# Performance work log

Measured on AMD Instinct MI355X. Metric: run time of the kernel, lower is better.

## Reference

```python
import jax, jax.numpy as jnp
import numpy as np

N_PTILES = 4096
MAX_SOURCES = 1
PTILE_SLEN = 53  # odd -> slen == ptile_slen, size_lens is identity
N_BANDS = 1


def setup_inputs() -> dict:
    key = jax.random.key(0)
    k1, k2, k3, k4, k5, k6 = jax.random.split(key, 6)
    shape = (N_PTILES, MAX_SOURCES)
    gal = jax.random.uniform(k1, shape + (7,), dtype=jnp.float32)
    # realistic SIE lens params per _sample_lens_params: b in [5,30], q in (0,1)
    b = jax.random.uniform(k2, shape + (1,), dtype=jnp.float32) * 25.0 + 5.0
    centers = jax.random.normal(k3, shape + (2,), dtype=jnp.float32)
    q = jax.random.uniform(k4, shape + (1,), dtype=jnp.float32) * 0.8 + 0.1
    beta = (jax.random.uniform(k5, shape + (1,), dtype=jnp.float32) - 0.5) * (np.pi / 2)
    ellf = (1.0 - q) / (1.0 + q)
    e1 = ellf * jnp.cos(beta)
    e2 = ellf * jnp.sin(beta)
    lens_params = jnp.concatenate([gal, b, centers, e1, e2], axis=-1)  # [..., 12]
    bools = (jax.random.uniform(k6, shape + (1,), dtype=jnp.float32) < 0.7).astype(jnp.float32)
    return {"lens_params": lens_params, "lensed_galaxy_bools": bools}


def _render_unlensed(gal_p, slen):
    # Differentiable Gaussian stand-in for the (CPU galsim) unlensed source render.
    c = jnp.arange(slen, dtype=jnp.float32) - (slen - 1) / 2.0
    yy, xx = jnp.meshgrid(c, c, indexing="ij")
    flux = gal_p[:, 0] * 1000.0 + 100.0      # [N]
    sigma = gal_p[:, 3] * 3.0 + 1.0          # [N]
    r2 = xx[None] ** 2 + yy[None] ** 2       # [1, S, S]
    s2 = (sigma ** 2)[:, None, None]
    return flux[:, None, None] * jnp.exp(-0.5 * r2 / s2) / (2.0 * np.pi * s2)


def _sie_deflection(x, y, lens_p):
    # x, y: [1, S, S]; lens_p: [N, 5] -> (xg, yg): [N, S, S]
    b, cx, cy, e1, e2 = [lens_p[:, i][:, None, None] for i in range(5)]
    ell = jnp.sqrt(e1 ** 2 + e2 ** 2)
    q = (1.0 - ell) / (1.0 + ell)
    phirad = jnp.arctan(e2 / e1)
    cosp, sinp = jnp.cos(phirad), jnp.sin(phirad)
    xsie = (x - cx) * cosp + (y - cy) * sinp
    ysie = (y - cy) * cosp - (x - cx) * sinp
    r_ell = jnp.sqrt(q * xsie ** 2 + ysie ** 2 / q + 1e-12)
    qfact = jnp.sqrt(1.0 / q - q)
    eps = 0.001
    safe = jnp.maximum(qfact, eps)
    denom = r_ell + (r_ell == 0)
    xtg = jnp.where(qfact >= eps, b / safe * jnp.arctan(safe * xsie / denom), b * xsie / denom)
    ytg = jnp.where(qfact >= eps, b / safe * jnp.arctanh(safe * ysie / denom), b * ysie / denom)
    xg = xtg * cosp - ytg * sinp
    yg = ytg * cosp + xtg * sinp
    return xg, yg


def _bilinear(im, xs, ys):
    # im: [N, S, S]; xs (col coord), ys (row coord): [N, S, S]
    N, S, _ = im.shape
    x0 = jnp.clip(jnp.floor(xs).astype(jnp.int32), 0, S - 1)
    x1 = jnp.clip(jnp.floor(xs).astype(jnp.int32) + 1, 0, S - 1)
    y0 = jnp.clip(jnp.floor(ys).astype(jnp.int32), 0, S - 1)
    y1 = jnp.clip(jnp.floor(ys).astype(jnp.int32) + 1, 0, S - 1)
    flat = im.reshape(N, S * S)

    def g(yi, xi):
        return jnp.take_along_axis(flat, (yi * S + xi).reshape(N, -1), axis=1).reshape(N, S, S)

    x0f, x1f = x0.astype(im.dtype), x1.astype(im.dtype)
    y0f, y1f = y0.astype(im.dtype), y1.astype(im.dtype)
    # weights use the CLIPPED integer corners, matching bilinear_interpolate_numpy
    wa = (x1f - xs) * (y1f - ys)
    wb = (x1f - xs) * (ys - y0f)
    wc = (xs - x0f) * (y1f - ys)
    wd = (xs - x0f) * (ys - y0f)
    return g(y0, x0) * wa + g(y1, x0) * wb + g(y0, x1) * wc + g(y1, x1) * wd


def _forward(lens_params, lensed_galaxy_bools):
    n_ptiles, max_s, P = lens_params.shape
    z = lens_params.reshape(-1, P)
    gal_p, lens_p = z[:, :7], z[:, 7:]
    slen = PTILE_SLEN
    unlensed = _render_unlensed(gal_p, slen)            # [N, S, S]
    # grid exactly as lens_galsim: range [-nx//2, nx//2] over nx points
    nx = slen
    lo = float((-nx) // 2)   # -27 for nx=53
    hi = float(nx // 2)      # 26
    coords = (hi - lo) * jnp.arange(nx, dtype=jnp.float32) / (nx - 1) + lo
    x = jnp.broadcast_to(coords[None, :], (nx, nx))  # varies along columns
    y = jnp.broadcast_to(coords[:, None], (nx, nx))  # varies along rows
    xg, yg = _sie_deflection(x[None], y[None], lens_p)
    shift = float(nx // 2)
    lensed = _bilinear(unlensed, x[None] - xg + shift, y[None] - yg + shift)
    out = lensed.reshape(n_ptiles, max_s, N_BANDS, slen, slen)
    # render-all + mask is equivalent to the zeros-init + boolean-fill + final mask
    return out * lensed_galaxy_bools[..., None, None]


def reference(lens_params, lensed_galaxy_bools):
    return _forward(lens_params, lensed_galaxy_bools)
```

## Files before the change

### kernel.cpp

```cpp
#include <hip/hip_runtime.h>
#include <math.h>

#define SLEN 53
#define NPIX 2809
#define NPARAM 12
#define BLK 256
#define NSLOT 11

__device__ __forceinline__ float fast_atan(float u) {
    float t = __builtin_fabsf(u);
    float rin = __builtin_amdgcn_rcpf(t);
    bool big = t > 1.0f;
    float w = big ? rin : t;
    float z = w * w;
    float p = -0.01172120f;
    p = __builtin_fmaf(p, z,  0.05265332f);
    p = __builtin_fmaf(p, z, -0.11643287f);
    p = __builtin_fmaf(p, z,  0.19354346f);
    p = __builtin_fmaf(p, z, -0.33262347f);
    p = __builtin_fmaf(p, z,  0.99997726f);
    float r = w * p;
    r = big ? 1.57079632679489662f - r : r;
    return __builtin_copysignf(r, u);
}

__device__ __forceinline__ float fast_atanh(float v) {
    float a = __builtin_fabsf(v);
    float t = (1.0f + a) * __builtin_amdgcn_rcpf(1.0f - a);
    float r = 0.34657359027997264f * __builtin_amdgcn_logf(t);
    return __builtin_copysignf(r, v);
}

__global__ __launch_bounds__(BLK) void lgtd_kernel(
    const float* __restrict__ lens_params,
    const float* __restrict__ bools,
    float* __restrict__ out)
{
    __shared__ float Etab[SLEN + 3];
    const int tile = blockIdx.x;
    float* outp = out + (size_t)tile * NPIX;
    const int tid = threadIdx.x;

    const float bl = bools[tile];
    if (bl == 0.0f) {
        #pragma unroll
        for (int s = 0; s < NSLOT; ++s) {
            const int idx = s * BLK + tid;
            if (s < NSLOT - 1 || idx < NPIX) outp[idx] = 0.0f;
        }
        return;
    }

    const float* p = lens_params + tile * NPARAM;
    const float flux = __builtin_fmaf(p[0], 1000.0f, 100.0f);
    const float sg   = __builtin_fmaf(p[3], 3.0f, 1.0f);
    const float s2   = sg * sg;
    const float rs2  = __builtin_amdgcn_rcpf(s2);
    const float A    = flux * 0.15915494309189533577f * rs2;
    const float nh2  = -0.72134752044448170368f * rs2;
    const float b  = p[7], cx = p[8], cy = p[9], e1 = p[10], e2 = p[11];
    const float rell = __builtin_amdgcn_rsqf(__builtin_fmaf(e1, e1, e2 * e2));
    const float cosp = e1 * rell;
    const float sinp = e2 * rell;
    const float ell  = __builtin_fmaf(e1, cosp, e2 * sinp);
    const float q    = (1.0f - ell) * __builtin_amdgcn_rcpf(1.0f + ell);
    const float qinv = __builtin_amdgcn_rcpf(q);
    const float qf   = __builtin_amdgcn_sqrtf(qinv - q);
    const float safe = fmaxf(qf, 0.001f);
    const float bos  = b * __builtin_amdgcn_rcpf(safe);
    const bool  mb   = (qf >= 0.001f);

    const float sA = __builtin_amdgcn_sqrtf(A * bl);
    if (tid < SLEN) {
        const float d = (float)tid - 26.0f;
        Etab[tid] = sA * __builtin_amdgcn_exp2f((nh2 * d) * d);
    }
    __syncthreads();

    const float KC = 1.019230769230769231f;
    #pragma unroll
    for (int s = 0; s < NSLOT; ++s) {
        int idx = s * BLK + tid;
        if (s == NSLOT - 1) idx = min(idx, NPIX - 1);
        const unsigned i = ((unsigned)idx * 39569u) >> 21;
        const int j = idx - (int)i * 53;
        const float xc = __builtin_fmaf((float)j, KC, -27.0f);
        const float yc = __builtin_fmaf((float)i, KC, -27.0f);

        const float dx = xc - cx, dy = yc - cy;
        const float xsie = __builtin_fmaf(dx, cosp, dy * sinp);
        const float ysie = __builtin_fmaf(dy, cosp, -dx * sinp);
        const float arg  = __builtin_fmaf(q * xsie, xsie,
                           __builtin_fmaf(qinv * ysie, ysie, 1e-12f));
        const float rcp_r = __builtin_amdgcn_rsqf(arg);
        float xtg, ytg;
        if (mb) {
            const float srr = safe * rcp_r;
            xtg = bos * fast_atan(srr * xsie);
            ytg = bos * fast_atanh(srr * ysie);
        } else {
            const float brr = b * rcp_r;
            xtg = brr * xsie;
            ytg = brr * ysie;
        }
        const float xg = __builtin_fmaf(xtg, cosp, -ytg * sinp);
        const float yg = __builtin_fmaf(ytg, cosp,  xtg * sinp);

        const float xs = (xc + 26.0f) - xg;
        const float ys = (yc + 26.0f) - yg;
        const float fx = __builtin_floorf(xs);
        const float fy = __builtin_floorf(ys);
        const float x0f = fminf(fmaxf(fx,        0.0f), 52.0f);
        const float x1f = fminf(fmaxf(fx + 1.0f, 0.0f), 52.0f);
        const float y0f = fminf(fmaxf(fy,        0.0f), 52.0f);
        const float y1f = fminf(fmaxf(fy + 1.0f, 0.0f), 52.0f);

        const float Ex0 = Etab[(int)x0f];
        const float Ex1 = Etab[(int)x1f];
        const float Ey0 = Etab[(int)y0f];
        const float Ey1 = Etab[(int)y1f];

        const float Fx = __builtin_fmaf(x1f - xs, Ex0, (xs - x0f) * Ex1);
        const float Fy = __builtin_fmaf(y1f - ys, Ey0, (ys - y0f) * Ey1);
        outp[idx] = Fx * Fy;
    }
}

extern "C" void kernel_launch(void* const* d_in, const int* in_sizes, int n_in,
                              void* d_out, int out_size, void* d_ws, size_t ws_size,
                              hipStream_t stream) {
    const float* lens  = (const float*)d_in[0];
    const float* bools = (const float*)d_in[1];
    float* out = (float*)d_out;
    const int n_tiles = in_sizes[1];
    lgtd_kernel<<<n_tiles, BLK, 0, stream>>>(lens, bools, out);
}
```

Baseline: 82.69 us.

## Process four tiles per block to amortize setup and share pixel coordinates

Each block now handles four tiles instead of one, with per-tile lens parameters held in register arrays and a four-row shared Gaussian table. The pixel index, row/column and coordinate math are computed once per pixel and reused across the four tiles. This cuts the block count fourfold and spreads per-block setup and sync over more work. In exchange the per-tile branch on zero masks moves inside the inner loop, the outer slot loop is no longer unrolled, register pressure rises, and fewer blocks are available to fill the GPU.

```diff
diff --git a/kernel.cpp b/kernel.cpp
--- a/kernel.cpp
+++ b/kernel.cpp
@@ -5,7 +5,9 @@
 #define NPIX 2809
 #define NPARAM 12
 #define BLK 256
+#define TPB 4
 #define NSLOT 11
+#define KC 1.019230769230769231f
 
 __device__ __forceinline__ float fast_atan(float u) {
     float t = __builtin_fabsf(u);
@@ -34,95 +36,132 @@
 __global__ __launch_bounds__(BLK) void lgtd_kernel(
     const float* __restrict__ lens_params,
     const float* __restrict__ bools,
-    float* __restrict__ out)
+    float* __restrict__ out, int n_tiles)
 {
-    __shared__ float Etab[SLEN + 3];
-    const int tile = blockIdx.x;
-    float* outp = out + (size_t)tile * NPIX;
+    __shared__ float Etab[TPB][SLEN];
+    const int base = blockIdx.x * TPB;
     const int tid = threadIdx.x;
 
-    const float bl = bools[tile];
-    if (bl == 0.0f) {
+    float blv[TPB];
+    bool  val[TPB];
+    bool  any = false;
+    #pragma unroll
+    for (int t = 0; t < TPB; ++t) {
+        val[t] = (base + t < n_tiles);
+        blv[t] = val[t] ? bools[base + t] : 0.0f;
+        any = any || (blv[t] != 0.0f);
+    }
+    if (!any) {
         #pragma unroll
-        for (int s = 0; s < NSLOT; ++s) {
-            const int idx = s * BLK + tid;
-            if (s < NSLOT - 1 || idx < NPIX) outp[idx] = 0.0f;
+        for (int t = 0; t < TPB; ++t) {
+            if (!val[t]) continue;
+            float* outp = out + (size_t)(base + t) * NPIX;
+            #pragma unroll 1
+            for (int s = 0; s < NSLOT; ++s)
+                outp[min(s * BLK + tid, NPIX - 1)] = 0.0f;
         }
         return;
     }
 
-    const float* p = lens_params + tile * NPARAM;
-    const float flux = __builtin_fmaf(p[0], 1000.0f, 100.0f);
-    const float sg   = __builtin_fmaf(p[3], 3.0f, 1.0f);
-    const float s2   = sg * sg;
-    const float rs2  = __builtin_amdgcn_rcpf(s2);
-    const float A    = flux * 0.15915494309189533577f * rs2;
-    const float nh2  = -0.72134752044448170368f * rs2;
-    const float b  = p[7], cx = p[8], cy = p[9], e1 = p[10], e2 = p[11];
-    const float rell = __builtin_amdgcn_rsqf(__builtin_fmaf(e1, e1, e2 * e2));
-    const float cosp = e1 * rell;
-    const float sinp = e2 * rell;
-    const float ell  = __builtin_fmaf(e1, cosp, e2 * sinp);
-    const float q    = (1.0f - ell) * __builtin_amdgcn_rcpf(1.0f + ell);
-    const float qinv = __builtin_amdgcn_rcpf(q);
-    const float qf   = __builtin_amdgcn_sqrtf(qinv - q);
-    const float safe = fmaxf(qf, 0.001f);
-    const float bos  = b * __builtin_amdgcn_rcpf(safe);
-    const bool  mb   = (qf >= 0.001f);
+    float cospv[TPB], sinpv[TPB], qv[TPB], qinvv[TPB], safev[TPB],
+          bosv[TPB], cxv[TPB], cyv[TPB], bv[TPB], nh2v[TPB], sAv[TPB];
+    bool  mbv[TPB];
+    #pragma unroll
+    for (int t = 0; t < TPB; ++t) {
+        if (blv[t] == 0.0f) {
+            cospv[t]=1.0f; sinpv[t]=0.0f; qv[t]=1.0f; qinvv[t]=1.0f;
+            safev[t]=1.0f; bosv[t]=0.0f; cxv[t]=0.0f; cyv[t]=0.0f;
+            bv[t]=0.0f; nh2v[t]=0.0f; sAv[t]=0.0f; mbv[t]=true;
+            continue;
+        }
+        const float* p = lens_params + (size_t)(base + t) * NPARAM;
+        const float flux = __builtin_fmaf(p[0], 1000.0f, 100.0f);
+        const float sg   = __builtin_fmaf(p[3], 3.0f, 1.0f);
+        const float s2   = sg * sg;
+        const float rs2  = __builtin_amdgcn_rcpf(s2);
+        const float A    = flux * 0.15915494309189533577f * rs2;
+        nh2v[t] = -0.72134752044448170368f * rs2;
+        bv[t] = p[7]; cxv[t] = p[8]; cyv[t] = p[9];
+        const float e1 = p[10], e2 = p[11];
+        const float rell = __builtin_amdgcn_rsqf(__builtin_fmaf(e1, e1, e2 * e2));
+        const float cosp = e1 * rell;
+        const float sinp = e2 * rell;
+        cospv[t] = cosp; sinpv[t] = sinp;
+        const float ell  = __builtin_fmaf(e1, cosp, e2 * sinp);
+        const float q    = (1.0f - ell) * __builtin_amdgcn_rcpf(1.0f + ell);
+        qv[t] = q;
+        const float qinv = __builtin_amdgcn_rcpf(q);
+        qinvv[t] = qinv;
+        const float qf   = __builtin_amdgcn_sqrtf(qinv - q);
+        const float safe = fmaxf(qf, 0.001f);
+        safev[t] = safe;
+        bosv[t]  = bv[t] * __builtin_amdgcn_rcpf(safe);
+        mbv[t]   = (qf >= 0.001f);
+        sAv[t]   = __builtin_amdgcn_sqrtf(A * blv[t]);
+    }
 
-    const float sA = __builtin_amdgcn_sqrtf(A * bl);
     if (tid < SLEN) {
-        const float d = (float)tid - 26.0f;
-        Etab[tid] = sA * __builtin_amdgcn_exp2f((nh2 * d) * d);
+        const float d  = (float)tid - 26.0f;
+        const float d2 = d * d;
+        #pragma unroll
+        for (int t = 0; t < TPB; ++t)
+            Etab[t][tid] = sAv[t] * __builtin_amdgcn_exp2f(nh2v[t] * d2);
     }
     __syncthreads();
 
-    const float KC = 1.019230769230769231f;
-    #pragma unroll
+    #pragma unroll 1
     for (int s = 0; s < NSLOT; ++s) {
-        int idx = s * BLK + tid;
-        if (s == NSLOT - 1) idx = min(idx, NPIX - 1);
+        const int idx = min(s * BLK + tid, NPIX - 1);
         const unsigned i = ((unsigned)idx * 39569u) >> 21;
         const int j = idx - (int)i * 53;
         const float xc = __builtin_fmaf((float)j, KC, -27.0f);
         const float yc = __builtin_fmaf((float)i, KC, -27.0f);
+        const float xs26 = xc + 26.0f;
+        const float ys26 = yc + 26.0f;
 
-        const float dx = xc - cx, dy = yc - cy;
-        const float xsie = __builtin_fmaf(dx, cosp, dy * sinp);
-        const float ysie = __builtin_fmaf(dy, cosp, -dx * sinp);
-        const float arg  = __builtin_fmaf(q * xsie, xsie,
-                           __builtin_fmaf(qinv * ysie, ysie, 1e-12f));
-        const float rcp_r = __builtin_amdgcn_rsqf(arg);
-        float xtg, ytg;
-        if (mb) {
-            const float srr = safe * rcp_r;
-            xtg = bos * fast_atan(srr * xsie);
-            ytg = bos * fast_atanh(srr * ysie);
-        } else {
-            const float brr = b * rcp_r;
-            xtg = brr * xsie;
-            ytg = brr * ysie;
+        #pragma unroll
+        for (int t = 0; t < TPB; ++t) {
+            if (!val[t]) continue;
+            float* outp = out + (size_t)(base + t) * NPIX + idx;
+            if (blv[t] == 0.0f) { *outp = 0.0f; continue; }
+
+            const float dx = xc - cxv[t], dy = yc - cyv[t];
+            const float xsie = __builtin_fmaf(dx, cospv[t], dy * sinpv[t]);
+            const float ysie = __builtin_fmaf(dy, cospv[t], -dx * sinpv[t]);
+            const float arg  = __builtin_fmaf(qv[t] * xsie, xsie,
+                               __builtin_fmaf(qinvv[t] * ysie, ysie, 1e-12f));
+            const float rcp_r = __builtin_amdgcn_rsqf(arg);
+            float xtg, ytg;
+            if (mbv[t]) {
+                const float srr = safev[t] * rcp_r;
+                xtg = bosv[t] * fast_atan(srr * xsie);
+                ytg = bosv[t] * fast_atanh(srr * ysie);
+            } else {
+                const float brr = bv[t] * rcp_r;
+                xtg = brr * xsie;
+                ytg = brr * ysie;
+            }
+            const float xg = __builtin_fmaf(xtg, cospv[t], -ytg * sinpv[t]);
+            const float yg = __builtin_fmaf(ytg, cospv[t],  xtg * sinpv[t]);
+
+            const float xs = xs26 - xg;
+            const float ys = ys26 - yg;
+            const float fx = __builtin_floorf(xs);
+            const float fy = __builtin_floorf(ys);
+            const float x0f = fminf(fmaxf(fx,        0.0f), 52.0f);
+            const float x1f = fminf(fmaxf(fx + 1.0f, 0.0f), 52.0f);
+            const float y0f = fminf(fmaxf(fy,        0.0f), 52.0f);
+            const float y1f = fminf(fmaxf(fy + 1.0f, 0.0f), 52.0f);
+
+            const float Ex0 = Etab[t][(int)x0f];
+            const float Ex1 = Etab[t][(int)x1f];
+            const float Ey0 = Etab[t][(int)y0f];
+            const float Ey1 = Etab[t][(int)y1f];
+
+            const float Fx = __builtin_fmaf(x1f - xs, Ex0, (xs - x0f) * Ex1);
+            const float Fy = __builtin_fmaf(y1f - ys, Ey0, (ys - y0f) * Ey1);
+            *outp = Fx * Fy;
         }
-        const float xg = __builtin_fmaf(xtg, cosp, -ytg * sinp);
-        const float yg = __builtin_fmaf(ytg, cosp,  xtg * sinp);
-
-        const float xs = (xc + 26.0f) - xg;
-        const float ys = (yc + 26.0f) - yg;
-        const float fx = __builtin_floorf(xs);
-        const float fy = __builtin_floorf(ys);
-        const float x0f = fminf(fmaxf(fx,        0.0f), 52.0f);
-        const float x1f = fminf(fmaxf(fx + 1.0f, 0.0f), 52.0f);
-        const float y0f = fminf(fmaxf(fy,        0.0f), 52.0f);
-        const float y1f = fminf(fmaxf(fy + 1.0f, 0.0f), 52.0f);
-
-        const float Ex0 = Etab[(int)x0f];
-        const float Ex1 = Etab[(int)x1f];
-        const float Ey0 = Etab[(int)y0f];
-        const float Ey1 = Etab[(int)y1f];
-
-        const float Fx = __builtin_fmaf(x1f - xs, Ex0, (xs - x0f) * Ex1);
-        const float Fy = __builtin_fmaf(y1f - ys, Ey0, (ys - y0f) * Ey1);
-        outp[idx] = Fx * Fy;
     }
 }
 
@@ -133,5 +172,6 @@
     const float* bools = (const float*)d_in[1];
     float* out = (float*)d_out;
     const int n_tiles = in_sizes[1];
-    lgtd_kernel<<<n_tiles, BLK, 0, stream>>>(lens, bools, out);
+    const int ngrp = (n_tiles + TPB - 1) / TPB;
+    lgtd_kernel<<<ngrp, BLK, 0, stream>>>(lens, bools, out, n_tiles);
 }
```

New measurement: 87.88 us. 1.06x slower.
